# Performance work log

Measured on AMD Instinct MI355X. Metric: run time of the kernel, lower is better.

## Reference

```python
import jax, jax.numpy as jnp
import numpy as np

L, H, P = 16384, 512, 512
DT_MIN, DT_MAX = 1e-3, 1e-1


def setup_inputs() -> dict:
    key = jax.random.key(0)
    ks = jax.random.split(key, 9)
    u = jax.random.normal(ks[0], (L, H), dtype=jnp.float32)
    # stable diagonal state matrix: Re(Lambda) < 0 (HiPPO-style init)
    Lambda_re = -(0.5 * jax.random.uniform(ks[1], (P,), dtype=jnp.float32) + 1e-3)
    Lambda_im = jnp.pi * jax.random.normal(ks[2], (P,), dtype=jnp.float32)
    # lecun-normal-ish scaling for B (fan-in H) and C (fan-in P)
    B_re = jax.random.normal(ks[3], (P, H), dtype=jnp.float32) / jnp.sqrt(2.0 * H)
    B_im = jax.random.normal(ks[4], (P, H), dtype=jnp.float32) / jnp.sqrt(2.0 * H)
    C_re = jax.random.normal(ks[5], (H, P), dtype=jnp.float32) / jnp.sqrt(2.0 * P)
    C_im = jax.random.normal(ks[6], (H, P), dtype=jnp.float32) / jnp.sqrt(2.0 * P)
    D = jax.random.uniform(ks[7], (H,), dtype=jnp.float32)
    # init_log_steps: uniform in [log(dt_min), log(dt_max)]
    lo, hi = np.log(DT_MIN), np.log(DT_MAX)
    log_step = jax.random.uniform(ks[8], (P,), dtype=jnp.float32, minval=lo, maxval=hi)
    return {"u": u, "Lambda_re": Lambda_re, "Lambda_im": Lambda_im,
            "B_re": B_re, "B_im": B_im, "C_re": C_re, "C_im": C_im,
            "D": D, "log_step": log_step}


def _binary_op(q_i, q_j):
    # associative combine for diagonal linear recurrence (elementwise over (L, P))
    A_i, b_i = q_i
    A_j, b_j = q_j
    return (A_j * A_i, A_j * b_i + b_j)


def reference(u, Lambda_re, Lambda_im, B_re, B_im, C_re, C_im, D, log_step):
    Lambda = Lambda_re + 1j * Lambda_im            # (P,) complex64
    B_tilde = B_re + 1j * B_im                     # (P, H)
    C_tilde = C_re + 1j * C_im                     # (H, P)
    step = jnp.exp(log_step)                       # (P,)
    # zero-order-hold discretization
    Lambda_bar = jnp.exp(Lambda * step)            # (P,)
    B_bar = ((Lambda_bar - 1.0) / Lambda)[:, None] * B_tilde  # (P, H)
    # Bu_t = B_bar @ u_t for all t, as one GEMM: (L, H) @ (H, P)
    Bu = u.astype(B_bar.dtype) @ B_bar.T           # (L, P) complex
    Lambda_el = jnp.broadcast_to(Lambda_bar, Bu.shape)  # (L, P)
    _, xs = jax.lax.associative_scan(_binary_op, (Lambda_el, Bu))  # xs: (L, P)
    # y_t = Re(C_tilde @ x_t) + D * u_t, batched as one GEMM
    ys = (xs @ C_tilde.T).real + D * u             # (L, H)
    return ys.astype(jnp.float32)
```

## Files before the change

### kernel.cpp

```cpp
#include <hip/hip_runtime.h>
#include <stdint.h>

#define L_DIM 16384
#define H_DIM 512
#define P_DIM 512
#define T_CH  32
#define NC    (L_DIM / T_CH)
#define LP    ((size_t)L_DIM * P_DIM)
#define LH    ((size_t)L_DIM * H_DIM)

typedef unsigned short u16;
typedef __attribute__((ext_vector_type(8))) _Float16 f16x8;
typedef __attribute__((ext_vector_type(4))) float f32x4;
typedef __attribute__((ext_vector_type(8))) unsigned short u16x8;

__device__ __forceinline__ u16 f2h(float x) {
    _Float16 h = (_Float16)x;
    return __builtin_bit_cast(u16, h);
}
__device__ __forceinline__ float h2f(u16 h) {
    return (float)__builtin_bit_cast(_Float16, h);
}

__device__ __forceinline__ void gload16(const void* g, void* lds) {
    __builtin_amdgcn_global_load_lds(
        (const __attribute__((address_space(1))) void*)g,
        (__attribute__((address_space(3))) void*)(uintptr_t)lds,
        16, 0, 0);
}

__device__ __forceinline__ f32x4 mfma_f16(f16x8 a, f16x8 b, f32x4 c) {
    return __builtin_amdgcn_mfma_f32_16x16x32_f16(a, b, c, 0, 0, 0);
}

__device__ __forceinline__ void zoh_lambda(
    const float* Lre, const float* Lim, const float* log_step, int p,
    float& lr, float& li)
{
    float st = expf(log_step[p]);
    float ar = Lre[p] * st, ai = Lim[p] * st;
    float er = expf(ar);
    lr = er * cosf(ai);
    li = er * sinf(ai);
}

__global__ __launch_bounds__(256) void front_kernel(
    const float* __restrict__ u,
    const float* __restrict__ Lre, const float* __restrict__ Lim,
    const float* __restrict__ log_step,
    const float* __restrict__ Bre, const float* __restrict__ Bim,
    const float* __restrict__ Cre, const float* __restrict__ Cim,
    u16* __restrict__ uh, u16* __restrict__ Bcat, u16* __restrict__ Ccat,
    float* __restrict__ lbr, float* __restrict__ lbi,
    float* __restrict__ powr, float* __restrict__ powi)
{
    int b = blockIdx.x;
    if (b < 4096) {
        size_t i = ((size_t)b * 256 + threadIdx.x) * 8;
        float4 v0 = *(const float4*)(u + i);
        float4 v1 = *(const float4*)(u + i + 4);
        u16x8 h;
        h[0] = f2h(v0.x); h[1] = f2h(v0.y); h[2] = f2h(v0.z); h[3] = f2h(v0.w);
        h[4] = f2h(v1.x); h[5] = f2h(v1.y); h[6] = f2h(v1.z); h[7] = f2h(v1.w);
        *(u16x8*)(uh + i) = h;
    } else if (b < 5120) {
        int idx = (b - 4096) * 256 + threadIdx.x;
        int p = idx >> 9, h = idx & 511;
        float lr, li;
        zoh_lambda(Lre, Lim, log_step, p, lr, li);
        float den = Lre[p] * Lre[p] + Lim[p] * Lim[p];
        float x = lr - 1.0f, y = li;
        float gr = (x * Lre[p] + y * Lim[p]) / den;
        float gi = (y * Lre[p] - x * Lim[p]) / den;
        float br = Bre[idx], bi = Bim[idx];
        Bcat[(size_t)p * 512 + h]         = f2h(gr * br - gi * bi);
        Bcat[(size_t)(512 + p) * 512 + h] = f2h(gr * bi + gi * br);
    } else if (b < 6144) {
        int idx = (b - 5120) * 256 + threadIdx.x;
        int h = idx >> 9, p = idx & 511;
        size_t row = (size_t)h * 1024;
        Ccat[row + p]       = f2h(Cre[idx]);
        Ccat[row + 512 + p] = f2h(-Cim[idx]);
    } else {
        #pragma unroll
        for (int t = 0; t < 2; ++t) {
            int p = threadIdx.x + t * 256;
            float lr, li;
            zoh_lambda(Lre, Lim, log_step, p, lr, li);
            lbr[p] = lr; lbi[p] = li;
            float pr = 1.f, pi2 = 0.f;
            powr[p] = 1.f; powi[p] = 0.f;
            for (int k = 1; k <= T_CH; ++k) {
                float nr = pr * lr - pi2 * li;
                float ni = pr * li + pi2 * lr;
                pr = nr; pi2 = ni;
                powr[(size_t)k * P_DIM + p] = pr;
                powi[(size_t)k * P_DIM + p] = pi2;
            }
        }
    }
}

__global__ __launch_bounds__(256, 2) void gemm_bu(
    const u16* __restrict__ A0,
    const u16* __restrict__ Bmat,
    u16* __restrict__ O0, u16* __restrict__ O1,
    const float* __restrict__ powr, const float* __restrict__ powi,
    float* __restrict__ Rwr, float* __restrict__ Rwi,
    float* __restrict__ Iwr, float* __restrict__ Iwi)
{
    const int NBN = 8;
    __shared__ u16 Als[2][128 * 64];
    __shared__ u16 Bls[2][128 * 64];

    int b = blockIdx.x;
    int m = (b & 7) * 16 + b / (8 * NBN);
    int n = (b >> 3) & (NBN - 1);
    int m0 = m * 128, n0 = n * 128;

    int tid = threadIdx.x;
    int w = tid >> 6, lane = tid & 63;
    int wm = w >> 1, wn = w & 1;

    f32x4 acc[4][4];
    #pragma unroll
    for (int i = 0; i < 4; ++i)
        #pragma unroll
        for (int j = 0; j < 4; ++j) acc[i][j] = (f32x4)0.f;

    int lr8  = lane >> 3;
    int slin = lane & 7;

    auto stage = [&](int kt, int buf) {
        int ko = kt * 64;
        char* Ad = (char*)&Als[buf][0];
        char* Bd = (char*)&Bls[buf][0];
        #pragma unroll
        for (int c = 0; c < 4; ++c) {
            int sidx = w * 4 + c;
            int r = sidx * 8 + lr8;
            int g = slin ^ (r & 7);
            gload16(A0   + (size_t)(m0 + r) * 512 + ko + g * 8, Ad + sidx * 1024);
            gload16(Bmat + (size_t)(n0 + r) * 512 + ko + g * 8, Bd + sidx * 1024);
        }
    };

    stage(0, 0);

    #pragma unroll
    for (int kt = 0; kt < 8; ++kt) {
        int cur = kt & 1;
        if (kt < 7) {
            stage(kt + 1, cur ^ 1);
            asm volatile("s_waitcnt vmcnt(8)" ::: "memory");
        } else {
            asm volatile("s_waitcnt vmcnt(0)" ::: "memory");
        }
        __builtin_amdgcn_s_barrier();
        __builtin_amdgcn_sched_barrier(0);

        char* AlsB = (char*)&Als[cur][0];
        char* BlsB = (char*)&Bls[cur][0];
        f16x8 a[4][2], bf[4][2];
        #pragma unroll
        for (int mm = 0; mm < 4; ++mm)
            #pragma unroll
            for (int kk = 0; kk < 2; ++kk) {
                int row = wm * 64 + mm * 16 + (lane & 15);
                int sl  = kk * 4 + (lane >> 4);
                int off = row * 128 + ((sl ^ (lane & 7)) << 4);
                a[mm][kk] = *(const f16x8*)(AlsB + off);
            }
        #pragma unroll
        for (int nn = 0; nn < 4; ++nn)
            #pragma unroll
            for (int kk = 0; kk < 2; ++kk) {
                int row = wn * 64 + nn * 16 + (lane & 15);
                int sl  = kk * 4 + (lane >> 4);
                int off = row * 128 + ((sl ^ (lane & 7)) << 4);
                bf[nn][kk] = *(const f16x8*)(BlsB + off);
            }
        #pragma unroll
        for (int mm = 0; mm < 4; ++mm)
            #pragma unroll
            for (int nn = 0; nn < 4; ++nn) {
                acc[mm][nn] = mfma_f16(a[mm][0], bf[nn][0], acc[mm][nn]);
                acc[mm][nn] = mfma_f16(a[mm][1], bf[nn][1], acc[mm][nn]);
            }

        __builtin_amdgcn_sched_barrier(0);
        __builtin_amdgcn_s_barrier();
    }

    int colb = n0 + wn * 64;
    int rowb = m0 + wm * 64;
    #pragma unroll
    for (int mm = 0; mm < 4; ++mm)
        #pragma unroll
        for (int nn = 0; nn < 4; ++nn) {
            f32x4 v = acc[mm][nn];
            int col = colb + nn * 16 + (lane & 15);
            #pragma unroll
            for (int j = 0; j < 4; ++j) {
                int row = rowb + mm * 16 + (lane >> 4) * 4 + j;
                size_t oidx = (size_t)row * 512 + (col & 511);
                u16 hv = f2h(v[j]);
                if (col < 512) O0[oidx] = hv;
                else           O1[oidx] = hv;
            }
        }

    float swr[2][4] = {{0.f}};
    float swi[2][4] = {{0.f}};
    #pragma unroll
    for (int h = 0; h < 2; ++h)
        #pragma unroll
        for (int j = 0; j < 4; ++j) {
            int k = h * 16 + (lane >> 4) * 4 + j;
            int e = (T_CH - 1) - k;
            #pragma unroll
            for (int nn = 0; nn < 4; ++nn) {
                int p = (colb + nn * 16 + (lane & 15)) & 511;
                float wr = powr[(size_t)e * 512 + p];
                float wi = powi[(size_t)e * 512 + p];
                swr[0][nn] = fmaf(wr, acc[h][nn][j],     swr[0][nn]);
                swi[0][nn] = fmaf(wi, acc[h][nn][j],     swi[0][nn]);
                swr[1][nn] = fmaf(wr, acc[2 + h][nn][j], swr[1][nn]);
                swi[1][nn] = fmaf(wi, acc[2 + h][nn][j], swi[1][nn]);
            }
        }
    #pragma unroll
    for (int ch = 0; ch < 2; ++ch)
        #pragma unroll
        for (int nn = 0; nn < 4; ++nn) {
            float a2 = swr[ch][nn];
            a2 += __shfl_xor(a2, 16); a2 += __shfl_xor(a2, 32);
            swr[ch][nn] = a2;
            float b2 = swi[ch][nn];
            b2 += __shfl_xor(b2, 16); b2 += __shfl_xor(b2, 32);
            swi[ch][nn] = b2;
        }
    if (lane < 16) {
        #pragma unroll
        for (int ch = 0; ch < 2; ++ch) {
            int c = (m0 >> 5) + wm * 2 + ch;
            #pragma unroll
            for (int nn = 0; nn < 4; ++nn) {
                int col = colb + nn * 16 + lane;
                int p = col & 511;
                size_t pidx = (size_t)c * 512 + p;
                if (col < 512) { Rwr[pidx] = swr[ch][nn]; Rwi[pidx] = swi[ch][nn]; }
                else           { Iwr[pidx] = swr[ch][nn]; Iwi[pidx] = swi[ch][nn]; }
            }
        }
    }
}

__global__ __launch_bounds__(64) void scan_chunks(
    const float* __restrict__ Rwr, const float* __restrict__ Rwi,
    const float* __restrict__ Iwr, const float* __restrict__ Iwi,
    const float* __restrict__ powr, const float* __restrict__ powi,
    float* __restrict__ carr, float* __restrict__ cari)
{
    int p = blockIdx.x * 64 + threadIdx.x;
    float ar = powr[(size_t)T_CH * P_DIM + p];
    float ai = powi[(size_t)T_CH * P_DIM + p];
    float sr = 0.f, si = 0.f;
    #pragma unroll 8
    for (int c = 0; c < NC; ++c) {
        size_t idx = (size_t)c * P_DIM + p;
        carr[idx] = sr; cari[idx] = si;
        float vre = Rwr[idx] - Iwi[idx];
        float vim = Rwi[idx] + Iwr[idx];
        float nr = fmaf(ar, sr, fmaf(-ai, si, vre));
        float ni = fmaf(ar, si, fmaf( ai, sr, vim));
        sr = nr; si = ni;
    }
}

__global__ __launch_bounds__(P_DIM) void scan_fix(
    const u16* __restrict__ burh, const u16* __restrict__ buih,
    const float* __restrict__ lbr, const float* __restrict__ lbi,
    const float* __restrict__ carr, const float* __restrict__ cari,
    u16* __restrict__ xrh, u16* __restrict__ xih)
{
    int p = threadIdx.x;
    int c = blockIdx.x;
    float lr = lbr[p], li = lbi[p];
    float xr = carr[(size_t)c * P_DIM + p];
    float xi = cari[(size_t)c * P_DIM + p];
    size_t base = (size_t)c * T_CH * P_DIM + p;
    #pragma unroll 4
    for (int k = 0; k < T_CH; ++k) {
        size_t idx = base + (size_t)k * P_DIM;
        float br = h2f(burh[idx]), bi = h2f(buih[idx]);
        float nr = fmaf(lr, xr, fmaf(-li, xi, br));
        float ni = fmaf(lr, xi, fmaf( li, xr, bi));
        xr = nr; xi = ni;
        xrh[idx] = f2h(xr);
        xih[idx] = f2h(xi);
    }
}

__global__ __launch_bounds__(256, 2) void gemm_y(
    const u16* __restrict__ A0, const u16* __restrict__ A1,
    const u16* __restrict__ Ccat,
    const float* __restrict__ Dvec, const u16* __restrict__ uIn,
    float* __restrict__ out)
{
    __shared__ u16 Als[2][128 * 64];
    __shared__ u16 Bls[2][128 * 64];

    int b = blockIdx.x;
    int m = (b & 7) * 16 + b / 32;
    int n = (b >> 3) & 3;
    int m0 = m * 128, n0 = n * 128;

    int tid = threadIdx.x;
    int w = tid >> 6, lane = tid & 63;
    int wm = w >> 1, wn = w & 1;

    f32x4 acc[4][4];
    #pragma unroll
    for (int i = 0; i < 4; ++i)
        #pragma unroll
        for (int j = 0; j < 4; ++j) acc[i][j] = (f32x4)0.f;

    int lr8  = lane >> 3;
    int slin = lane & 7;

    auto stage = [&](int kt, int buf) {
        const u16* Ap = (kt < 8) ? A0 : A1;
        int ko = (kt & 7) * 64;
        int kB = kt * 64;
        char* Ad = (char*)&Als[buf][0];
        char* Bd = (char*)&Bls[buf][0];
        #pragma unroll
        for (int c = 0; c < 4; ++c) {
            int sidx = w * 4 + c;
            int r = sidx * 8 + lr8;
            int g = slin ^ (r & 7);
            gload16(Ap   + (size_t)(m0 + r) * 512  + ko + g * 8, Ad + sidx * 1024);
            gload16(Ccat + (size_t)(n0 + r) * 1024 + kB + g * 8, Bd + sidx * 1024);
        }
    };

    stage(0, 0);

    #pragma unroll
    for (int kt = 0; kt < 16; ++kt) {
        int cur = kt & 1;
        if (kt < 15) {
            stage(kt + 1, cur ^ 1);
            asm volatile("s_waitcnt vmcnt(8)" ::: "memory");
        } else {
            asm volatile("s_waitcnt vmcnt(0)" ::: "memory");
        }
        __builtin_amdgcn_s_barrier();
        __builtin_amdgcn_sched_barrier(0);

        char* AlsB = (char*)&Als[cur][0];
        char* BlsB = (char*)&Bls[cur][0];
        f16x8 a[4][2], bf[4][2];
        #pragma unroll
        for (int mm = 0; mm < 4; ++mm)
            #pragma unroll
            for (int kk = 0; kk < 2; ++kk) {
                int row = wm * 64 + mm * 16 + (lane & 15);
                int sl  = kk * 4 + (lane >> 4);
                int off = row * 128 + ((sl ^ (lane & 7)) << 4);
                a[mm][kk] = *(const f16x8*)(AlsB + off);
            }
        #pragma unroll
        for (int nn = 0; nn < 4; ++nn)
            #pragma unroll
            for (int kk = 0; kk < 2; ++kk) {
                int row = wn * 64 + nn * 16 + (lane & 15);
                int sl  = kk * 4 + (lane >> 4);
                int off = row * 128 + ((sl ^ (lane & 7)) << 4);
                bf[nn][kk] = *(const f16x8*)(BlsB + off);
            }
        #pragma unroll
        for (int mm = 0; mm < 4; ++mm)
            #pragma unroll
            for (int nn = 0; nn < 4; ++nn) {
                acc[mm][nn] = mfma_f16(a[mm][0], bf[nn][0], acc[mm][nn]);
                acc[mm][nn] = mfma_f16(a[mm][1], bf[nn][1], acc[mm][nn]);
            }

        __builtin_amdgcn_sched_barrier(0);
        __builtin_amdgcn_s_barrier();
    }

    int colb = n0 + wn * 64;
    int rowb = m0 + wm * 64;
    #pragma unroll
    for (int mm = 0; mm < 4; ++mm)
        #pragma unroll
        for (int nn = 0; nn < 4; ++nn) {
            f32x4 v = acc[mm][nn];
            int col = colb + nn * 16 + (lane & 15);
            #pragma unroll
            for (int j = 0; j < 4; ++j) {
                int row = rowb + mm * 16 + (lane >> 4) * 4 + j;
                size_t oidx = (size_t)row * 512 + col;
                out[oidx] = v[j] + Dvec[col] * h2f(uIn[oidx]);
            }
        }
}

extern "C" void kernel_launch(void* const* d_in, const int* in_sizes, int n_in,
                              void* d_out, int out_size, void* d_ws, size_t ws_size,
                              hipStream_t stream)
{
    const float* u        = (const float*)d_in[0];
    const float* Lre      = (const float*)d_in[1];
    const float* Lim      = (const float*)d_in[2];
    const float* Bre      = (const float*)d_in[3];
    const float* Bim      = (const float*)d_in[4];
    const float* Cre      = (const float*)d_in[5];
    const float* Cim      = (const float*)d_in[6];
    const float* D        = (const float*)d_in[7];
    const float* log_step = (const float*)d_in[8];
    float* out = (float*)d_out;

    char* w8 = (char*)d_ws;
    u16*   burh = (u16*)(w8);
    u16*   buih = (u16*)(w8 + 16777216);
    u16*   xrh  = (u16*)(w8 + 33554432);
    u16*   xih  = (u16*)(w8 + 50331648);
    u16*   uh   = (u16*)(w8 + 67108864);
    u16*   Bcat = (u16*)(w8 + 83886080);
    u16*   Ccat = (u16*)(w8 + 84934656);
    float* Rwr  = (float*)(w8 + 85983232);
    float* Rwi  = (float*)(w8 + 87031808);
    float* Iwr  = (float*)(w8 + 88080384);
    float* Iwi  = (float*)(w8 + 89128960);
    float* carr = (float*)(w8 + 90177536);
    float* cari = (float*)(w8 + 91226112);
    float* powr = (float*)(w8 + 92274688);
    float* powi = (float*)(w8 + 92342272);
    float* lbr  = (float*)(w8 + 92409856);
    float* lbi  = lbr + P_DIM;

    front_kernel<<<6145, 256, 0, stream>>>(
        u, Lre, Lim, log_step, Bre, Bim, Cre, Cim,
        uh, Bcat, Ccat, lbr, lbi, powr, powi);

    gemm_bu<<<1024, 256, 0, stream>>>(
        uh, Bcat, burh, buih, powr, powi, Rwr, Rwi, Iwr, Iwi);

    scan_chunks<<<8, 64, 0, stream>>>(Rwr, Rwi, Iwr, Iwi, powr, powi, carr, cari);
    scan_fix<<<NC, P_DIM, 0, stream>>>(burh, buih, lbr, lbi, carr, cari, xrh, xih);

    gemm_y<<<512, 256, 0, stream>>>(xrh, xih, Ccat, D, uh, out);
}
```

Before: 111.7 us.

## Interleave real and imaginary parts across Bu, scan state and C layouts

Reorders the B_bar rows and C_tilde columns so the real and imaginary components of each state p sit next to each other. The Bu GEMM output, the per-chunk summaries, the carries and the scanned states then live in single interleaved buffers. scan_fix now does one 32-bit load and one 32-bit store per element instead of two 16-bit accesses, and scan_chunks reads one float2 instead of four separate arrays. The intent is to cut memory transactions and the branchy split stores in the scan kernels. In exchange, the GEMM epilogue needs an extra shuffle to combine lane pairs and a select per weight.

```diff
diff --git a/kernel.cpp b/kernel.cpp
--- a/kernel.cpp
+++ b/kernel.cpp
@@ -32,6 +32,7 @@
 __device__ __forceinline__ f32x4 mfma_f16(f16x8 a, f16x8 b, f32x4 c) {
     return __builtin_amdgcn_mfma_f32_16x16x32_f16(a, b, c, 0, 0, 0);
 }
+
 
 __device__ __forceinline__ void zoh_lambda(
     const float* Lre, const float* Lim, const float* log_step, int p,
@@ -73,14 +74,13 @@
         float gr = (x * Lre[p] + y * Lim[p]) / den;
         float gi = (y * Lre[p] - x * Lim[p]) / den;
         float br = Bre[idx], bi = Bim[idx];
-        Bcat[(size_t)p * 512 + h]         = f2h(gr * br - gi * bi);
-        Bcat[(size_t)(512 + p) * 512 + h] = f2h(gr * bi + gi * br);
+        Bcat[(size_t)(2 * p) * 512 + h]     = f2h(gr * br - gi * bi);
+        Bcat[(size_t)(2 * p + 1) * 512 + h] = f2h(gr * bi + gi * br);
     } else if (b < 6144) {
         int idx = (b - 5120) * 256 + threadIdx.x;
         int h = idx >> 9, p = idx & 511;
-        size_t row = (size_t)h * 1024;
-        Ccat[row + p]       = f2h(Cre[idx]);
-        Ccat[row + 512 + p] = f2h(-Cim[idx]);
+        uint32_t pk = (uint32_t)f2h(Cre[idx]) | ((uint32_t)f2h(-Cim[idx]) << 16);
+        *(uint32_t*)(Ccat + (size_t)h * 1024 + 2 * p) = pk;
     } else {
         #pragma unroll
         for (int t = 0; t < 2; ++t) {
@@ -104,10 +104,9 @@
 __global__ __launch_bounds__(256, 2) void gemm_bu(
     const u16* __restrict__ A0,
     const u16* __restrict__ Bmat,
-    u16* __restrict__ O0, u16* __restrict__ O1,
+    u16* __restrict__ Ou,
     const float* __restrict__ powr, const float* __restrict__ powi,
-    float* __restrict__ Rwr, float* __restrict__ Rwi,
-    float* __restrict__ Iwr, float* __restrict__ Iwi)
+    float* __restrict__ scf)
 {
     const int NBN = 8;
     __shared__ u16 Als[2][128 * 64];
@@ -203,15 +202,12 @@
             #pragma unroll
             for (int j = 0; j < 4; ++j) {
                 int row = rowb + mm * 16 + (lane >> 4) * 4 + j;
-                size_t oidx = (size_t)row * 512 + (col & 511);
-                u16 hv = f2h(v[j]);
-                if (col < 512) O0[oidx] = hv;
-                else           O1[oidx] = hv;
-            }
-        }
-
-    float swr[2][4] = {{0.f}};
-    float swi[2][4] = {{0.f}};
+                Ou[(size_t)row * 1024 + col] = f2h(v[j]);
+            }
+        }
+
+    float s1[2][4] = {{0.f}};
+    float s2[2][4] = {{0.f}};
     #pragma unroll
     for (int h = 0; h < 2; ++h)
         #pragma unroll
@@ -220,25 +216,28 @@
             int e = (T_CH - 1) - k;
             #pragma unroll
             for (int nn = 0; nn < 4; ++nn) {
-                int p = (colb + nn * 16 + (lane & 15)) & 511;
+                int col = colb + nn * 16 + (lane & 15);
+                int p = col >> 1, sel = col & 1;
                 float wr = powr[(size_t)e * 512 + p];
                 float wi = powi[(size_t)e * 512 + p];
-                swr[0][nn] = fmaf(wr, acc[h][nn][j],     swr[0][nn]);
-                swi[0][nn] = fmaf(wi, acc[h][nn][j],     swi[0][nn]);
-                swr[1][nn] = fmaf(wr, acc[2 + h][nn][j], swr[1][nn]);
-                swi[1][nn] = fmaf(wi, acc[2 + h][nn][j], swi[1][nn]);
+                float w1 = sel ? -wi : wr;
+                float w2 = sel ?  wr : wi;
+                s1[0][nn] = fmaf(w1, acc[h][nn][j],     s1[0][nn]);
+                s2[0][nn] = fmaf(w2, acc[h][nn][j],     s2[0][nn]);
+                s1[1][nn] = fmaf(w1, acc[2 + h][nn][j], s1[1][nn]);
+                s2[1][nn] = fmaf(w2, acc[2 + h][nn][j], s2[1][nn]);
             }
         }
     #pragma unroll
     for (int ch = 0; ch < 2; ++ch)
         #pragma unroll
         for (int nn = 0; nn < 4; ++nn) {
-            float a2 = swr[ch][nn];
-            a2 += __shfl_xor(a2, 16); a2 += __shfl_xor(a2, 32);
-            swr[ch][nn] = a2;
-            float b2 = swi[ch][nn];
-            b2 += __shfl_xor(b2, 16); b2 += __shfl_xor(b2, 32);
-            swi[ch][nn] = b2;
+            float a2 = s1[ch][nn];
+            a2 += __shfl_xor(a2, 1); a2 += __shfl_xor(a2, 16); a2 += __shfl_xor(a2, 32);
+            s1[ch][nn] = a2;
+            float b2 = s2[ch][nn];
+            b2 += __shfl_xor(b2, 1); b2 += __shfl_xor(b2, 16); b2 += __shfl_xor(b2, 32);
+            s2[ch][nn] = b2;
         }
     if (lane < 16) {
         #pragma unroll
@@ -247,20 +246,16 @@
             #pragma unroll
             for (int nn = 0; nn < 4; ++nn) {
                 int col = colb + nn * 16 + lane;
-                int p = col & 511;
-                size_t pidx = (size_t)c * 512 + p;
-                if (col < 512) { Rwr[pidx] = swr[ch][nn]; Rwi[pidx] = swi[ch][nn]; }
-                else           { Iwr[pidx] = swr[ch][nn]; Iwi[pidx] = swi[ch][nn]; }
+                scf[(size_t)c * 1024 + col] = (col & 1) ? s2[ch][nn] : s1[ch][nn];
             }
         }
     }
 }
 
 __global__ __launch_bounds__(64) void scan_chunks(
-    const float* __restrict__ Rwr, const float* __restrict__ Rwi,
-    const float* __restrict__ Iwr, const float* __restrict__ Iwi,
+    const float* __restrict__ scf,
     const float* __restrict__ powr, const float* __restrict__ powi,
-    float* __restrict__ carr, float* __restrict__ cari)
+    float* __restrict__ carrci)
 {
     int p = blockIdx.x * 64 + threadIdx.x;
     float ar = powr[(size_t)T_CH * P_DIM + p];
@@ -268,42 +263,43 @@
     float sr = 0.f, si = 0.f;
     #pragma unroll 8
     for (int c = 0; c < NC; ++c) {
-        size_t idx = (size_t)c * P_DIM + p;
-        carr[idx] = sr; cari[idx] = si;
-        float vre = Rwr[idx] - Iwi[idx];
-        float vim = Rwi[idx] + Iwr[idx];
-        float nr = fmaf(ar, sr, fmaf(-ai, si, vre));
-        float ni = fmaf(ar, si, fmaf( ai, sr, vim));
+        size_t idx = ((size_t)c * 512 + p) * 2;
+        float2 cv; cv.x = sr; cv.y = si;
+        *(float2*)(carrci + idx) = cv;
+        float2 sv = *(const float2*)(scf + idx);
+        float nr = fmaf(ar, sr, fmaf(-ai, si, sv.x));
+        float ni = fmaf(ar, si, fmaf( ai, sr, sv.y));
         sr = nr; si = ni;
     }
 }
 
 __global__ __launch_bounds__(P_DIM) void scan_fix(
-    const u16* __restrict__ burh, const u16* __restrict__ buih,
+    const uint32_t* __restrict__ buc,
     const float* __restrict__ lbr, const float* __restrict__ lbi,
-    const float* __restrict__ carr, const float* __restrict__ cari,
-    u16* __restrict__ xrh, u16* __restrict__ xih)
+    const float* __restrict__ carrci,
+    uint32_t* __restrict__ xc)
 {
     int p = threadIdx.x;
     int c = blockIdx.x;
     float lr = lbr[p], li = lbi[p];
-    float xr = carr[(size_t)c * P_DIM + p];
-    float xi = cari[(size_t)c * P_DIM + p];
-    size_t base = (size_t)c * T_CH * P_DIM + p;
-    #pragma unroll 4
+    float2 cv = *(const float2*)(carrci + ((size_t)c * 512 + p) * 2);
+    float xr = cv.x, xi = cv.y;
+    size_t base = (size_t)c * T_CH * 512 + p;
+    #pragma unroll 8
     for (int k = 0; k < T_CH; ++k) {
-        size_t idx = base + (size_t)k * P_DIM;
-        float br = h2f(burh[idx]), bi = h2f(buih[idx]);
+        size_t idx = base + (size_t)k * 512;
+        uint32_t bv = buc[idx];
+        float br = h2f((u16)(bv & 0xffffu));
+        float bi = h2f((u16)(bv >> 16));
         float nr = fmaf(lr, xr, fmaf(-li, xi, br));
         float ni = fmaf(lr, xi, fmaf( li, xr, bi));
         xr = nr; xi = ni;
-        xrh[idx] = f2h(xr);
-        xih[idx] = f2h(xi);
+        xc[idx] = (uint32_t)f2h(nr) | ((uint32_t)f2h(ni) << 16);
     }
 }
 
 __global__ __launch_bounds__(256, 2) void gemm_y(
-    const u16* __restrict__ A0, const u16* __restrict__ A1,
+    const u16* __restrict__ Ax,
     const u16* __restrict__ Ccat,
     const float* __restrict__ Dvec, const u16* __restrict__ uIn,
     float* __restrict__ out)
@@ -330,8 +326,6 @@
     int slin = lane & 7;
 
     auto stage = [&](int kt, int buf) {
-        const u16* Ap = (kt < 8) ? A0 : A1;
-        int ko = (kt & 7) * 64;
         int kB = kt * 64;
         char* Ad = (char*)&Als[buf][0];
         char* Bd = (char*)&Bls[buf][0];
@@ -340,7 +334,7 @@
             int sidx = w * 4 + c;
             int r = sidx * 8 + lr8;
             int g = slin ^ (r & 7);
-            gload16(Ap   + (size_t)(m0 + r) * 512  + ko + g * 8, Ad + sidx * 1024);
+            gload16(Ax   + (size_t)(m0 + r) * 1024 + kB + g * 8, Ad + sidx * 1024);
             gload16(Ccat + (size_t)(n0 + r) * 1024 + kB + g * 8, Bd + sidx * 1024);
         }
     };
@@ -425,33 +419,27 @@
     float* out = (float*)d_out;
 
     char* w8 = (char*)d_ws;
-    u16*   burh = (u16*)(w8);
-    u16*   buih = (u16*)(w8 + 16777216);
-    u16*   xrh  = (u16*)(w8 + 33554432);
-    u16*   xih  = (u16*)(w8 + 50331648);
-    u16*   uh   = (u16*)(w8 + 67108864);
-    u16*   Bcat = (u16*)(w8 + 83886080);
-    u16*   Ccat = (u16*)(w8 + 84934656);
-    float* Rwr  = (float*)(w8 + 85983232);
-    float* Rwi  = (float*)(w8 + 87031808);
-    float* Iwr  = (float*)(w8 + 88080384);
-    float* Iwi  = (float*)(w8 + 89128960);
-    float* carr = (float*)(w8 + 90177536);
-    float* cari = (float*)(w8 + 91226112);
-    float* powr = (float*)(w8 + 92274688);
-    float* powi = (float*)(w8 + 92342272);
-    float* lbr  = (float*)(w8 + 92409856);
-    float* lbi  = lbr + P_DIM;
+    u16*      buc  = (u16*)(w8);
+    u16*      xc   = (u16*)(w8 + 33554432);
+    u16*      uh   = (u16*)(w8 + 67108864);
+    u16*      Bcat = (u16*)(w8 + 83886080);
+    u16*      Ccat = (u16*)(w8 + 84934656);
+    float*    scf  = (float*)(w8 + 85983232);
+    float*    carrci = (float*)(w8 + 88080384);
+    float*    powr = (float*)(w8 + 90177536);
+    float*    powi = (float*)(w8 + 90245120);
+    float*    lbr  = (float*)(w8 + 90312704);
+    float*    lbi  = lbr + P_DIM;
 
     front_kernel<<<6145, 256, 0, stream>>>(
         u, Lre, Lim, log_step, Bre, Bim, Cre, Cim,
         uh, Bcat, Ccat, lbr, lbi, powr, powi);
 
     gemm_bu<<<1024, 256, 0, stream>>>(
-        uh, Bcat, burh, buih, powr, powi, Rwr, Rwi, Iwr, Iwi);
-
-    scan_chunks<<<8, 64, 0, stream>>>(Rwr, Rwi, Iwr, Iwi, powr, powi, carr, cari);
-    scan_fix<<<NC, P_DIM, 0, stream>>>(burh, buih, lbr, lbi, carr, cari, xrh, xih);
-
-    gemm_y<<<512, 256, 0, stream>>>(xrh, xih, Ccat, D, uh, out);
-}
+        uh, Bcat, buc, powr, powi, scf);
+
+    scan_chunks<<<8, 64, 0, stream>>>(scf, powr, powi, carrci);
+    scan_fix<<<NC, P_DIM, 0, stream>>>((const uint32_t*)buc, lbr, lbi, carrci, (uint32_t*)xc);
+
+    gemm_y<<<512, 256, 0, stream>>>(xc, Ccat, D, uh, out);
+}
```

Result: faster. 106.0 us (-5.2%).
